# Performance work log

Measured on AMD Instinct MI355X. Metric: run time of the kernel, lower is better.

Reference implementation:

```python
import jax, jax.numpy as jnp
import numpy as np

B, L, Z, G = 512, 2713, 58, 8  # batch, chem features, seq len (zeta), d_model (gamma)
H, HD, FF, NL = 8, 1, 2048, 6  # heads, head_dim, ffn dim, layers
RNA_IN, LIN1, LIN2 = 1018, 256, 64
CAT, C1, C2 = LIN2 + Z * G, 64, 8  # 528, 64, 8


def setup_inputs() -> dict:
    key = jax.random.key(0)
    ks = iter(jax.random.split(key, 40))
    r = lambda shape, s=0.05: (jax.random.normal(next(ks), shape, dtype=jnp.float32) * s)
    inp = {
        'rna': jax.random.normal(next(ks), (B, RNA_IN), dtype=jnp.float32),
        'drug': jax.random.normal(next(ks), (B, L, Z), dtype=jnp.float32),
        'lin1_w': r((LIN1, RNA_IN)), 'lin1_b': r((LIN1,)),
        'lin2_w': r((LIN2, LIN1)), 'lin2_b': r((LIN2,)),
        'chem_w': r((G, L)),  # chem_embedding: Linear(2713->8, no bias)
        'pos_w': r((G, Z)),   # pos_embedding on one-hot == its weight columns
        'qkv_w': r((NL, 3 * G, G)), 'qkv_b': r((NL, 3 * G)),
        'out_w': r((NL, G, G)), 'out_b': r((NL, G)),
        'ln1_g': jnp.ones((NL, G), jnp.float32), 'ln1_b': jnp.zeros((NL, G), jnp.float32),
        'ff1_w': r((NL, FF, G)), 'ff1_b': r((NL, FF)),
        'ff2_w': r((NL, G, FF)), 'ff2_b': r((NL, G)),
        'ln2_g': jnp.ones((NL, G), jnp.float32), 'ln2_b': jnp.zeros((NL, G), jnp.float32),
        'c1_w': r((C1, CAT)), 'c1_b': r((C1,)),
        'c2_w': r((C2, C1)), 'c2_b': r((C2,)),
        'c3_w': r((1, C2)), 'c3_b': r((1,)),
    }
    return inp


def _layernorm(x, g, b, eps=1e-5):
    mu = jnp.mean(x, axis=-1, keepdims=True)
    var = jnp.mean(jnp.square(x - mu), axis=-1, keepdims=True)
    return (x - mu) * jax.lax.rsqrt(var + eps) * g + b


def _forward(rna, drug, lin1_w, lin1_b, lin2_w, lin2_b, chem_w, pos_w,
             qkv_w, qkv_b, out_w, out_b, ln1_g, ln1_b,
             ff1_w, ff1_b, ff2_w, ff2_b, ln2_g, ln2_b,
             c1_w, c1_b, c2_w, c2_b, c3_w, c3_b):
    # rna branch: two linear layers (no activation in original forward)
    r = rna @ lin1_w.T + lin1_b
    r = r @ lin2_w.T + lin2_b  # [B, 64]

    # Embedding: E = W_chem @ M + W_pos (the double loop, vectorized)
    E = jnp.einsum('gl,blz->bgz', chem_w, drug) + pos_w[None]  # [B, G, Z]
    x = jnp.transpose(E, (0, 2, 1))  # [B, Z, G] (batch_first transformer input)

    scale = 1.0 / np.sqrt(HD)
    for i in range(NL):  # 6 post-norm TransformerEncoderLayers, relu FFN
        qkv = x @ qkv_w[i].T + qkv_b[i]  # [B, Z, 3G]
        q, k, v = jnp.split(qkv, 3, axis=-1)
        qh = q.reshape(B, Z, H, HD)
        kh = k.reshape(B, Z, H, HD)
        vh = v.reshape(B, Z, H, HD)
        scores = jnp.einsum('bshd,bthd->bhst', qh, kh) * scale
        a = jax.nn.softmax(scores, axis=-1)
        o = jnp.einsum('bhst,bthd->bshd', a, vh).reshape(B, Z, G)
        o = o @ out_w[i].T + out_b[i]
        x = _layernorm(x + o, ln1_g[i], ln1_b[i])
        ff = jax.nn.relu(x @ ff1_w[i].T + ff1_b[i]) @ ff2_w[i].T + ff2_b[i]
        x = _layernorm(x + ff, ln2_g[i], ln2_b[i])

    flat = x.reshape(B, Z * G)  # [B, 464]
    h = jnp.concatenate([r, flat], axis=1)  # [B, 528]
    h = h @ c1_w.T + c1_b
    h = h @ c2_w.T + c2_b
    return h @ c3_w.T + c3_b  # [B, 1]


def reference(rna, drug, lin1_w, lin1_b, lin2_w, lin2_b, chem_w, pos_w,
              qkv_w, qkv_b, out_w, out_b, ln1_g, ln1_b,
              ff1_w, ff1_b, ff2_w, ff2_b, ln2_g, ln2_b,
              c1_w, c1_b, c2_w, c2_b, c3_w, c3_b):
    return _forward(rna, drug, lin1_w, lin1_b, lin2_w, lin2_b, chem_w, pos_w,
                    qkv_w, qkv_b, out_w, out_b, ln1_g, ln1_b,
                    ff1_w, ff1_b, ff2_w, ff2_b, ln2_g, ln2_b,
                    c1_w, c1_b, c2_w, c2_b, c3_w, c3_b)
```

## Files before the change

### kernel.cpp

```cpp
#include <hip/hip_runtime.h>

#define BB 512
#define LDIM 2713
#define ZDIM 58
#define GDIM 8
#define NLAYER 6
#define FFDIM 2048
#define RNAIN 1018
#define CATDIM 528
#define NCAT 1482
#define LQ 679

typedef float v2f __attribute__((ext_vector_type(2)));
typedef float f32x4 __attribute__((ext_vector_type(4)));
typedef _Float16 f16x4 __attribute__((ext_vector_type(4)));

#define OFF_WCATT  0
#define OFF_BPRIME 94848

__global__ __launch_bounds__(1024) void prep_kernel(
    const float* __restrict__ lin1_w, const float* __restrict__ lin1_b,
    const float* __restrict__ lin2_w, const float* __restrict__ lin2_b,
    const float* __restrict__ c1_w, const float* __restrict__ c1_b,
    float* __restrict__ ws) {
    __shared__ float Tm[16384];
    const int t = threadIdx.x;
    float* WcatT = ws + OFF_WCATT;

    if (blockIdx.x == 16) {
        if (t < 64) {
            float a = lin2_b[t];
            #pragma unroll 4
            for (int n = 0; n < 256; ++n) a += lin2_w[t * 256 + n] * lin1_b[n];
            Tm[t] = a;
        }
        __syncthreads();
        if (t < 64) {
            float a = c1_b[t];
            #pragma unroll 4
            for (int m = 0; m < 64; ++m) a += c1_w[t * CATDIM + m] * Tm[m];
            ws[OFF_BPRIME + t] = a;
        }
        for (int i = t; i < 464 * 64; i += 1024) {
            int kk = i >> 6, j = i & 63;
            WcatT[(RNAIN + kk) * 64 + j] = c1_w[j * CATDIM + 64 + kk];
        }
        return;
    }

    for (int i = t; i < 16384; i += 1024) {
        int n = i >> 6, j = i & 63;
        float a = 0.f;
        #pragma unroll 8
        for (int m = 0; m < 64; ++m) a += c1_w[j * CATDIM + m] * lin2_w[m * 256 + n];
        Tm[i] = a;
    }
    __syncthreads();
    const int k0 = blockIdx.x * 64;
    const int j = t & 63;
    for (int kr = t >> 6; kr < 64; kr += 16) {
        int k = k0 + kr;
        if (k >= RNAIN) break;
        float a = 0.f;
        #pragma unroll 8
        for (int n = 0; n < 256; ++n) a += Tm[n * 64 + j] * lin1_w[n * RNAIN + k];
        WcatT[k * 64 + j] = a;
    }
}

__global__ __launch_bounds__(1024, 8) void mega_kernel(
    const float* __restrict__ drug, const float* __restrict__ chem_w,
    const float* __restrict__ pos_w,
    const float* __restrict__ ff1_w, const float* __restrict__ ff2_w,
    const float* __restrict__ ff1_b,
    const float* __restrict__ qkv_w, const float* __restrict__ qkv_b,
    const float* __restrict__ out_w, const float* __restrict__ out_b,
    const float* __restrict__ ln1_g, const float* __restrict__ ln1_b,
    const float* __restrict__ ff2_b,
    const float* __restrict__ ln2_g, const float* __restrict__ ln2_b,
    const float* __restrict__ rna, const float* __restrict__ WcatT,
    const float* __restrict__ bprime,
    const float* __restrict__ c2_w, const float* __restrict__ c2_b,
    const float* __restrict__ c3_w, const float* __restrict__ c3_b,
    float* __restrict__ out) {
    __shared__ float smem[12864];
    float* cwl    = smem;
    float* part_e = smem + 5440;
    float* xs    = smem;
    float* qs    = smem + 512;
    float* ks    = smem + 992;
    float* vs    = smem + 1472;
    float* os    = smem + 1952;
    float* part  = smem + 2464;
    float* qkvws = smem + 10656;
    float* qkvbs = smem + 11808;
    float* outws = smem + 11952;
    float* outbs = smem + 12336;
    float* l1gs  = smem + 12384;
    float* l1bs  = smem + 12432;
    float* l2gs  = smem + 12480;
    float* l2bs  = smem + 12528;
    float* f2bs  = smem + 12576;
    float* h1s   = smem + 12624;
    float* h2s   = smem + 12688;

    const int b = blockIdx.x;
    const int t = threadIdx.x;
    const int w = __builtin_amdgcn_readfirstlane(t >> 6);
    const int lane = t & 63;
    const int quad = lane >> 4;
    const int i16 = lane & 15;

    {
        const int zc = (lane < ZDIM) ? lane : (ZDIM - 1);
        v2f acc0 = {0.f, 0.f}, acc1 = {0.f, 0.f}, acc2 = {0.f, 0.f}, acc3 = {0.f, 0.f};
        for (int q = 0; q < 4; ++q) {
            const int l0 = q * LQ;
            const int nrows = (LDIM - l0 < LQ) ? (LDIM - l0) : LQ;
            __syncthreads();
            #pragma unroll
            for (int g = 0; g < 8; ++g)
                for (int i = t; i < nrows; i += 1024)
                    cwl[i * 8 + g] = chem_w[g * LDIM + l0 + i];
            __syncthreads();
            const float* dp = drug + (size_t)b * (LDIM * ZDIM) + (size_t)l0 * ZDIM;
            int r0 = w * 43;
            int r1 = (r0 + 43 < nrows) ? (r0 + 43) : nrows;
            int r = r0;
            for (; r + 4 <= r1; r += 4) {
                float d0 = dp[(r + 0) * ZDIM + zc];
                float d1 = dp[(r + 1) * ZDIM + zc];
                float d2 = dp[(r + 2) * ZDIM + zc];
                float d3 = dp[(r + 3) * ZDIM + zc];
                const v2f* c0 = (const v2f*)(cwl + (r + 0) * 8);
                const v2f* c1 = (const v2f*)(cwl + (r + 1) * 8);
                const v2f* c2 = (const v2f*)(cwl + (r + 2) * 8);
                const v2f* c3 = (const v2f*)(cwl + (r + 3) * 8);
                v2f dd;
                dd = (v2f){d0, d0};
                acc0 += c0[0] * dd; acc1 += c0[1] * dd; acc2 += c0[2] * dd; acc3 += c0[3] * dd;
                dd = (v2f){d1, d1};
                acc0 += c1[0] * dd; acc1 += c1[1] * dd; acc2 += c1[2] * dd; acc3 += c1[3] * dd;
                dd = (v2f){d2, d2};
                acc0 += c2[0] * dd; acc1 += c2[1] * dd; acc2 += c2[2] * dd; acc3 += c2[3] * dd;
                dd = (v2f){d3, d3};
                acc0 += c3[0] * dd; acc1 += c3[1] * dd; acc2 += c3[2] * dd; acc3 += c3[3] * dd;
            }
            for (; r < r1; ++r) {
                float d = dp[r * ZDIM + zc];
                const v2f* cc = (const v2f*)(cwl + r * 8);
                v2f dd = {d, d};
                acc0 += cc[0] * dd; acc1 += cc[1] * dd; acc2 += cc[2] * dd; acc3 += cc[3] * dd;
            }
        }
        if (lane < ZDIM) {
            v2f* pr = (v2f*)(part_e + w * 464 + zc * 8);
            pr[0] = acc0; pr[1] = acc1; pr[2] = acc2; pr[3] = acc3;
        }
        __syncthreads();
        if (t < 512) {
            if (t < 464) {
                int z = t >> 3, g = t & 7;
                float s = pos_w[g * ZDIM + z];
                #pragma unroll
                for (int ww = 0; ww < 16; ++ww) s += part_e[ww * 464 + t];
                xs[t] = s;
            } else {
                xs[t] = 0.f;
            }
        }
        __syncthreads();
    }

    for (int i = t; i < 1152; i += 1024) qkvws[i] = qkv_w[i];
    if (t < 144) qkvbs[t] = qkv_b[t];
    if (t < 384) outws[t] = out_w[t];
    if (t < 48) {
        outbs[t] = out_b[t];
        l1gs[t] = ln1_g[t]; l1bs[t] = ln1_b[t];
        l2gs[t] = ln2_g[t]; l2bs[t] = ln2_b[t];
        f2bs[t] = ff2_b[t];
    }
    __syncthreads();

    for (int li = 0; li < NLAYER; ++li) {
        if (t < 464) {
            int z = t >> 3, h = t & 7;
            const float4* xr = (const float4*)(xs + z * 8);
            float4 x0 = xr[0], x1 = xr[1];
            #pragma unroll
            for (int p = 0; p < 3; ++p) {
                int j = p * 8 + h;
                const float4* wr = (const float4*)(qkvws + li * 192 + j * 8);
                float4 w0 = wr[0], w1 = wr[1];
                float a = qkvbs[li * 24 + j]
                        + x0.x * w0.x + x0.y * w0.y + x0.z * w0.z + x0.w * w0.w
                        + x1.x * w1.x + x1.y * w1.y + x1.z * w1.z + x1.w * w1.w;
                float* dst = (p == 0) ? qs : (p == 1) ? ks : vs;
                dst[h * 60 + z] = a;
            }
        }
        __syncthreads();

        if (t < 464) {
            int h = t & 7, s = t >> 3;
            float q = qs[h * 60 + s];
            const float4* kr = (const float4*)(ks + h * 60);
            const float4* vr = (const float4*)(vs + h * 60);
            float sum = 0.f, oa = 0.f;
            #pragma unroll 2
            for (int c = 0; c < 14; ++c) {
                float4 k4 = kr[c], v4 = vr[c];
                float e0 = __expf(q * k4.x); sum += e0; oa += e0 * v4.x;
                float e1 = __expf(q * k4.y); sum += e1; oa += e1 * v4.y;
                float e2 = __expf(q * k4.z); sum += e2; oa += e2 * v4.z;
                float e3 = __expf(q * k4.w); sum += e3; oa += e3 * v4.w;
            }
            {
                const float* kk = ks + h * 60;
                const float* vv = vs + h * 60;
                float e0 = __expf(q * kk[56]); sum += e0; oa += e0 * vv[56];
                float e1 = __expf(q * kk[57]); sum += e1; oa += e1 * vv[57];
            }
            os[t] = oa / sum;
        }
        __syncthreads();

        if (t < 464) {
            int z = t >> 3, g = t & 7;
            const float4* orow = (const float4*)(os + z * 8);
            float4 o0 = orow[0], o1 = orow[1];
            const float4* wr = (const float4*)(outws + li * 64 + g * 8);
            float4 w0 = wr[0], w1 = wr[1];
            float a = outbs[li * 8 + g] + xs[t]
                    + o0.x * w0.x + o0.y * w0.y + o0.z * w0.z + o0.w * w0.w
                    + o1.x * w1.x + o1.y * w1.y + o1.z * w1.z + o1.w * w1.w;
            float s8 = a + __shfl_xor(a, 1);
            s8 += __shfl_xor(s8, 2);
            s8 += __shfl_xor(s8, 4);
            float mu = s8 * 0.125f;
            float d = a - mu;
            float vv = d * d;
            vv += __shfl_xor(vv, 1); vv += __shfl_xor(vv, 2); vv += __shfl_xor(vv, 4);
            float inv = rsqrtf(vv * 0.125f + 1e-5f);
            xs[t] = d * inv * l1gs[li * 8 + g] + l1bs[li * 8 + g];
        }
        __syncthreads();

        {
            f16x4 xb[4];
            #pragma unroll
            for (int nt = 0; nt < 4; ++nt) {
                if (quad < 2) {
                    const float4* xp = (const float4*)(xs + (nt * 16 + i16) * 8 + quad * 4);
                    float4 xv = *xp;
                    xb[nt][0] = (_Float16)xv.x; xb[nt][1] = (_Float16)xv.y;
                    xb[nt][2] = (_Float16)xv.z; xb[nt][3] = (_Float16)xv.w;
                } else {
                    xb[nt][0] = (_Float16)0.f; xb[nt][1] = (_Float16)0.f;
                    xb[nt][2] = (_Float16)0.f; xb[nt][3] = (_Float16)0.f;
                }
            }
            f32x4 oacc[4];
            #pragma unroll
            for (int nt = 0; nt < 4; ++nt) { oacc[nt][0]=0.f; oacc[nt][1]=0.f; oacc[nt][2]=0.f; oacc[nt][3]=0.f; }

            const float* w1p = ff1_w + ((size_t)li * FFDIM + w * 128) * 8;
            const float* a2p = ff2_w + (size_t)li * GDIM * FFDIM + w * 128;
            const float* b1p = ff1_b + li * FFDIM + w * 128;

            #pragma unroll 2
            for (int ft = 0; ft < 8; ++ft) {
                f16x4 w1f = {};
                if (lane < 32) {
                    f32x4 v = *(const f32x4*)(w1p + (size_t)(ft * 16 + i16) * 8 + quad * 4);
                    w1f[0] = (_Float16)v[0]; w1f[1] = (_Float16)v[1];
                    w1f[2] = (_Float16)v[2]; w1f[3] = (_Float16)v[3];
                }
                f16x4 a2f = {};
                if (i16 < 8) {
                    f32x4 v = *(const f32x4*)(a2p + (size_t)i16 * FFDIM + ft * 16 + quad * 4);
                    a2f[0] = (_Float16)v[0]; a2f[1] = (_Float16)v[1];
                    a2f[2] = (_Float16)v[2]; a2f[3] = (_Float16)v[3];
                }
                f32x4 b1v = *(const f32x4*)(b1p + ft * 16 + quad * 4);
                #pragma unroll
                for (int nt = 0; nt < 4; ++nt) {
                    f32x4 h = b1v;
                    h = __builtin_amdgcn_mfma_f32_16x16x16f16(w1f, xb[nt], h, 0, 0, 0);
                    h[0] = fmaxf(h[0], 0.f); h[1] = fmaxf(h[1], 0.f);
                    h[2] = fmaxf(h[2], 0.f); h[3] = fmaxf(h[3], 0.f);
                    f16x4 hb;
                    hb[0] = (_Float16)h[0]; hb[1] = (_Float16)h[1];
                    hb[2] = (_Float16)h[2]; hb[3] = (_Float16)h[3];
                    oacc[nt] = __builtin_amdgcn_mfma_f32_16x16x16f16(a2f, hb, oacc[nt], 0, 0, 0);
                }
            }
            if (quad < 2) {
                #pragma unroll
                for (int nt = 0; nt < 4; ++nt) {
                    float4 o4 = make_float4(oacc[nt][0], oacc[nt][1], oacc[nt][2], oacc[nt][3]);
                    *(float4*)(part + ((w * 64 + nt * 16 + i16) * 8 + quad * 4)) = o4;
                }
            }
        }
        __syncthreads();

        if (t < 464) {
            int z = t >> 3, g = t & 7;
            float s = 0.f;
            #pragma unroll
            for (int ww = 0; ww < 16; ++ww) s += part[(ww * 64 + z) * 8 + g];
            float a = xs[t] + s + f2bs[li * 8 + g];
            float s8 = a + __shfl_xor(a, 1);
            s8 += __shfl_xor(s8, 2);
            s8 += __shfl_xor(s8, 4);
            float mu = s8 * 0.125f;
            float d = a - mu;
            float vv = d * d;
            vv += __shfl_xor(vv, 1); vv += __shfl_xor(vv, 2); vv += __shfl_xor(vv, 4);
            float inv = rsqrtf(vv * 0.125f + 1e-5f);
            xs[t] = d * inv * l2gs[li * 8 + g] + l2bs[li * 8 + g];
        }
        __syncthreads();
    }

    {
        float* cat = part;
        float* partial = part + 4096;
        const float* rg = rna + (size_t)b * RNAIN;
        for (int i = t; i < RNAIN; i += 1024) cat[i] = rg[i];
        __syncthreads();
        int j = lane;
        int k0 = w * 93;
        int k1 = (k0 + 93 < NCAT) ? (k0 + 93) : NCAT;
        float a = (w == 0) ? bprime[j] : 0.f;
        #pragma unroll 4
        for (int k = k0; k < k1; ++k) {
            float ck = (k < RNAIN) ? cat[k] : xs[k - RNAIN];
            a += ck * WcatT[k * 64 + j];
        }
        partial[w * 64 + j] = a;
        __syncthreads();
        if (t < 64) {
            float s = 0.f;
            #pragma unroll
            for (int ww = 0; ww < 16; ++ww) s += partial[ww * 64 + t];
            h1s[t] = s;
        }
    }
    __syncthreads();
    if (t < 8) {
        float a2 = c2_b[t];
        #pragma unroll 8
        for (int m = 0; m < 64; ++m) a2 += h1s[m] * c2_w[t * 64 + m];
        h2s[t] = a2;
    }
    __syncthreads();
    if (t == 0) {
        float a3 = c3_b[0];
        #pragma unroll
        for (int jj = 0; jj < 8; ++jj) a3 += h2s[jj] * c3_w[jj];
        out[b] = a3;
    }
}

extern "C" void kernel_launch(void* const* d_in, const int* in_sizes, int n_in,
                              void* d_out, int out_size, void* d_ws, size_t ws_size,
                              hipStream_t stream) {
    const float* rna    = (const float*)d_in[0];
    const float* drug   = (const float*)d_in[1];
    const float* lin1_w = (const float*)d_in[2];
    const float* lin1_b = (const float*)d_in[3];
    const float* lin2_w = (const float*)d_in[4];
    const float* lin2_b = (const float*)d_in[5];
    const float* chem_w = (const float*)d_in[6];
    const float* pos_w  = (const float*)d_in[7];
    const float* qkv_w  = (const float*)d_in[8];
    const float* qkv_b  = (const float*)d_in[9];
    const float* out_w  = (const float*)d_in[10];
    const float* out_b  = (const float*)d_in[11];
    const float* ln1_g  = (const float*)d_in[12];
    const float* ln1_b  = (const float*)d_in[13];
    const float* ff1_w  = (const float*)d_in[14];
    const float* ff1_b  = (const float*)d_in[15];
    const float* ff2_w  = (const float*)d_in[16];
    const float* ff2_b  = (const float*)d_in[17];
    const float* ln2_g  = (const float*)d_in[18];
    const float* ln2_b  = (const float*)d_in[19];
    const float* c1_w   = (const float*)d_in[20];
    const float* c1_b   = (const float*)d_in[21];
    const float* c2_w   = (const float*)d_in[22];
    const float* c2_b   = (const float*)d_in[23];
    const float* c3_w   = (const float*)d_in[24];
    const float* c3_b   = (const float*)d_in[25];
    float* ws  = (float*)d_ws;
    float* out = (float*)d_out;

    hipLaunchKernelGGL(prep_kernel, dim3(17), dim3(1024), 0, stream,
                       lin1_w, lin1_b, lin2_w, lin2_b, c1_w, c1_b, ws);
    hipLaunchKernelGGL(mega_kernel, dim3(BB), dim3(1024), 0, stream,
                       drug, chem_w, pos_w, ff1_w, ff2_w, ff1_b,
                       qkv_w, qkv_b, out_w, out_b,
                       ln1_g, ln1_b, ff2_b, ln2_g, ln2_b,
                       rna, ws + OFF_WCATT, ws + OFF_BPRIME,
                       c2_w, c2_b, c3_w, c3_b, out);
}
```

Baseline: 732.6 us.

## Halve mega_kernel block size, fuse out-proj via shuffles, restructure prep GEMMs

The main kernel now runs with 512 threads per block instead of 1024, so each wave covers twice as many embedding rows, FFN tiles and classifier inputs, and shared memory shrinks so more blocks may fit per CU. The attention output projection is folded into the softmax threads with width-8 shuffles, which removes the os buffer and one barrier per layer. The prep kernel reorders its matrix product chain: it stages an lin1 tile and a transposed c1 in shared memory and computes lin2·lin1 first. The bias path is parallelised across threads. The trade-off is more serial work per wave in the main kernel in exchange for fewer barriers and possibly higher occupancy.

Result: faster. 698.9 us (-4.6%).

```diff
diff --git a/kernel.cpp b/kernel.cpp
--- a/kernel.cpp
+++ b/kernel.cpp
@@ -23,52 +23,76 @@
     const float* __restrict__ lin2_w, const float* __restrict__ lin2_b,
     const float* __restrict__ c1_w, const float* __restrict__ c1_b,
     float* __restrict__ ws) {
-    __shared__ float Tm[16384];
+    __shared__ float lin1s[256 * 64];
+    __shared__ float Ut[64 * 64];
+    __shared__ float c1T[64 * 64];
     const int t = threadIdx.x;
     float* WcatT = ws + OFF_WCATT;
 
     if (blockIdx.x == 16) {
+        {
+            int m = t >> 4, q = t & 15;
+            float a = 0.f;
+            #pragma unroll
+            for (int nn = 0; nn < 16; ++nn)
+                a += lin2_w[m * 256 + q * 16 + nn] * lin1_b[q * 16 + nn];
+            lin1s[m * 16 + q] = a;
+        }
+        __syncthreads();
         if (t < 64) {
             float a = lin2_b[t];
-            #pragma unroll 4
-            for (int n = 0; n < 256; ++n) a += lin2_w[t * 256 + n] * lin1_b[n];
-            Tm[t] = a;
+            #pragma unroll
+            for (int q = 0; q < 16; ++q) a += lin1s[t * 16 + q];
+            Ut[t] = a;
         }
         __syncthreads();
         if (t < 64) {
             float a = c1_b[t];
-            #pragma unroll 4
-            for (int m = 0; m < 64; ++m) a += c1_w[t * CATDIM + m] * Tm[m];
+            #pragma unroll 8
+            for (int m = 0; m < 64; ++m) a += c1_w[t * CATDIM + m] * Ut[m];
             ws[OFF_BPRIME + t] = a;
         }
         for (int i = t; i < 464 * 64; i += 1024) {
-            int kk = i >> 6, j = i & 63;
+            int j = i / 464, kk = i % 464;
             WcatT[(RNAIN + kk) * 64 + j] = c1_w[j * CATDIM + 64 + kk];
         }
         return;
     }
 
-    for (int i = t; i < 16384; i += 1024) {
-        int n = i >> 6, j = i & 63;
+    const int k0 = blockIdx.x * 64;
+    const int nk = (RNAIN - k0 < 64) ? (RNAIN - k0) : 64;
+    for (int i = t; i < 256 * 64; i += 1024) {
+        int n = i >> 6, kl = i & 63;
+        lin1s[i] = (kl < nk) ? lin1_w[n * RNAIN + k0 + kl] : 0.f;
+    }
+    for (int i = t; i < 64 * 64; i += 1024) {
+        int j = i >> 6, m = i & 63;
+        c1T[m * 64 + j] = c1_w[j * CATDIM + m];
+    }
+    __syncthreads();
+    for (int mp = 0; mp < 4; ++mp) {
+        int m = (t >> 6) + mp * 16;
+        int kl = t & 63;
+        const float* l2r = lin2_w + m * 256;
         float a = 0.f;
         #pragma unroll 8
-        for (int m = 0; m < 64; ++m) a += c1_w[j * CATDIM + m] * lin2_w[m * 256 + n];
-        Tm[i] = a;
+        for (int n = 0; n < 256; ++n) a += l2r[n] * lin1s[n * 64 + kl];
+        Ut[m * 64 + kl] = a;
     }
     __syncthreads();
-    const int k0 = blockIdx.x * 64;
-    const int j = t & 63;
-    for (int kr = t >> 6; kr < 64; kr += 16) {
-        int k = k0 + kr;
-        if (k >= RNAIN) break;
-        float a = 0.f;
-        #pragma unroll 8
-        for (int n = 0; n < 256; ++n) a += Tm[n * 64 + j] * lin1_w[n * RNAIN + k];
-        WcatT[k * 64 + j] = a;
+    for (int kp = 0; kp < 4; ++kp) {
+        int kr = (t >> 6) + kp * 16;
+        int j = t & 63;
+        if (kr < nk) {
+            float a = 0.f;
+            #pragma unroll 8
+            for (int m = 0; m < 64; ++m) a += Ut[m * 64 + kr] * c1T[m * 64 + j];
+            WcatT[(k0 + kr) * 64 + j] = a;
+        }
     }
 }
 
-__global__ __launch_bounds__(1024, 8) void mega_kernel(
+__global__ __launch_bounds__(512, 8) void mega_kernel(
     const float* __restrict__ drug, const float* __restrict__ chem_w,
     const float* __restrict__ pos_w,
     const float* __restrict__ ff1_w, const float* __restrict__ ff2_w,
@@ -83,26 +107,25 @@
     const float* __restrict__ c2_w, const float* __restrict__ c2_b,
     const float* __restrict__ c3_w, const float* __restrict__ c3_b,
     float* __restrict__ out) {
-    __shared__ float smem[12864];
+    __shared__ float smem[9152];
     float* cwl    = smem;
     float* part_e = smem + 5440;
     float* xs    = smem;
     float* qs    = smem + 512;
     float* ks    = smem + 992;
     float* vs    = smem + 1472;
-    float* os    = smem + 1952;
-    float* part  = smem + 2464;
-    float* qkvws = smem + 10656;
-    float* qkvbs = smem + 11808;
-    float* outws = smem + 11952;
-    float* outbs = smem + 12336;
-    float* l1gs  = smem + 12384;
-    float* l1bs  = smem + 12432;
-    float* l2gs  = smem + 12480;
-    float* l2bs  = smem + 12528;
-    float* f2bs  = smem + 12576;
-    float* h1s   = smem + 12624;
-    float* h2s   = smem + 12688;
+    float* part  = smem + 1952;
+    float* qkvws = smem + 6048;
+    float* qkvbs = smem + 7200;
+    float* outws = smem + 7344;
+    float* outbs = smem + 7728;
+    float* l1gs  = smem + 7776;
+    float* l1bs  = smem + 7824;
+    float* l2gs  = smem + 7872;
+    float* l2bs  = smem + 7920;
+    float* f2bs  = smem + 7968;
+    float* h1s   = smem + 8016;
+    float* h2s   = smem + 8080;
 
     const int b = blockIdx.x;
     const int t = threadIdx.x;
@@ -120,12 +143,12 @@
             __syncthreads();
             #pragma unroll
             for (int g = 0; g < 8; ++g)
-                for (int i = t; i < nrows; i += 1024)
+                for (int i = t; i < nrows; i += 512)
                     cwl[i * 8 + g] = chem_w[g * LDIM + l0 + i];
             __syncthreads();
             const float* dp = drug + (size_t)b * (LDIM * ZDIM) + (size_t)l0 * ZDIM;
-            int r0 = w * 43;
-            int r1 = (r0 + 43 < nrows) ? (r0 + 43) : nrows;
+            int r0 = w * 85;
+            int r1 = (r0 + 85 < nrows) ? (r0 + 85) : nrows;
             int r = r0;
             for (; r + 4 <= r1; r += 4) {
                 float d0 = dp[(r + 0) * ZDIM + zc];
@@ -158,21 +181,19 @@
             pr[0] = acc0; pr[1] = acc1; pr[2] = acc2; pr[3] = acc3;
         }
         __syncthreads();
-        if (t < 512) {
-            if (t < 464) {
-                int z = t >> 3, g = t & 7;
-                float s = pos_w[g * ZDIM + z];
-                #pragma unroll
-                for (int ww = 0; ww < 16; ++ww) s += part_e[ww * 464 + t];
-                xs[t] = s;
-            } else {
-                xs[t] = 0.f;
-            }
-        }
-        __syncthreads();
-    }
-
-    for (int i = t; i < 1152; i += 1024) qkvws[i] = qkv_w[i];
+        if (t < 464) {
+            int z = t >> 3, g = t & 7;
+            float s = pos_w[g * ZDIM + z];
+            #pragma unroll
+            for (int ww = 0; ww < 8; ++ww) s += part_e[ww * 464 + t];
+            xs[t] = s;
+        } else if (t < 512) {
+            xs[t] = 0.f;
+        }
+        __syncthreads();
+    }
+
+    for (int i = t; i < 1152; i += 512) qkvws[i] = qkv_w[i];
     if (t < 144) qkvbs[t] = qkv_b[t];
     if (t < 384) outws[t] = out_w[t];
     if (t < 48) {
@@ -222,19 +243,13 @@
                 float e0 = __expf(q * kk[56]); sum += e0; oa += e0 * vv[56];
                 float e1 = __expf(q * kk[57]); sum += e1; oa += e1 * vv[57];
             }
-            os[t] = oa / sum;
-        }
-        __syncthreads();
-
-        if (t < 464) {
-            int z = t >> 3, g = t & 7;
-            const float4* orow = (const float4*)(os + z * 8);
-            float4 o0 = orow[0], o1 = orow[1];
-            const float4* wr = (const float4*)(outws + li * 64 + g * 8);
-            float4 w0 = wr[0], w1 = wr[1];
-            float a = outbs[li * 8 + g] + xs[t]
-                    + o0.x * w0.x + o0.y * w0.y + o0.z * w0.z + o0.w * w0.w
-                    + o1.x * w1.x + o1.y * w1.y + o1.z * w1.z + o1.w * w1.w;
+            float o = oa / sum;
+            int g = h;
+            float a = outbs[li * 8 + g] + xs[t];
+            const float* wr8 = outws + li * 64 + g * 8;
+            #pragma unroll
+            for (int hh = 0; hh < 8; ++hh)
+                a += __shfl(o, hh, 8) * wr8[hh];
             float s8 = a + __shfl_xor(a, 1);
             s8 += __shfl_xor(s8, 2);
             s8 += __shfl_xor(s8, 4);
@@ -265,12 +280,12 @@
             #pragma unroll
             for (int nt = 0; nt < 4; ++nt) { oacc[nt][0]=0.f; oacc[nt][1]=0.f; oacc[nt][2]=0.f; oacc[nt][3]=0.f; }
 
-            const float* w1p = ff1_w + ((size_t)li * FFDIM + w * 128) * 8;
-            const float* a2p = ff2_w + (size_t)li * GDIM * FFDIM + w * 128;
-            const float* b1p = ff1_b + li * FFDIM + w * 128;
+            const float* w1p = ff1_w + ((size_t)li * FFDIM + w * 256) * 8;
+            const float* a2p = ff2_w + (size_t)li * GDIM * FFDIM + w * 256;
+            const float* b1p = ff1_b + li * FFDIM + w * 256;
 
             #pragma unroll 2
-            for (int ft = 0; ft < 8; ++ft) {
+            for (int ft = 0; ft < 16; ++ft) {
                 f16x4 w1f = {};
                 if (lane < 32) {
                     f32x4 v = *(const f32x4*)(w1p + (size_t)(ft * 16 + i16) * 8 + quad * 4);
@@ -310,7 +325,7 @@
             int z = t >> 3, g = t & 7;
             float s = 0.f;
             #pragma unroll
-            for (int ww = 0; ww < 16; ++ww) s += part[(ww * 64 + z) * 8 + g];
+            for (int ww = 0; ww < 8; ++ww) s += part[(ww * 64 + z) * 8 + g];
             float a = xs[t] + s + f2bs[li * 8 + g];
             float s8 = a + __shfl_xor(a, 1);
             s8 += __shfl_xor(s8, 2);
@@ -327,13 +342,13 @@
 
     {
         float* cat = part;
-        float* partial = part + 4096;
+        float* partial = part + 1024;
         const float* rg = rna + (size_t)b * RNAIN;
-        for (int i = t; i < RNAIN; i += 1024) cat[i] = rg[i];
+        for (int i = t; i < RNAIN; i += 512) cat[i] = rg[i];
         __syncthreads();
         int j = lane;
-        int k0 = w * 93;
-        int k1 = (k0 + 93 < NCAT) ? (k0 + 93) : NCAT;
+        int k0 = w * 186;
+        int k1 = (k0 + 186 < NCAT) ? (k0 + 186) : NCAT;
         float a = (w == 0) ? bprime[j] : 0.f;
         #pragma unroll 4
         for (int k = k0; k < k1; ++k) {
@@ -345,7 +360,7 @@
         if (t < 64) {
             float s = 0.f;
             #pragma unroll
-            for (int ww = 0; ww < 16; ++ww) s += partial[ww * 64 + t];
+            for (int ww = 0; ww < 8; ++ww) s += partial[ww * 64 + t];
             h1s[t] = s;
         }
     }
@@ -399,7 +414,7 @@
 
     hipLaunchKernelGGL(prep_kernel, dim3(17), dim3(1024), 0, stream,
                        lin1_w, lin1_b, lin2_w, lin2_b, c1_w, c1_b, ws);
-    hipLaunchKernelGGL(mega_kernel, dim3(BB), dim3(1024), 0, stream,
+    hipLaunchKernelGGL(mega_kernel, dim3(BB), dim3(512), 0, stream,
                        drug, chem_w, pos_w, ff1_w, ff2_w, ff1_b,
                        qkv_w, qkv_b, out_w, out_b,
                        ln1_g, ln1_b, ff2_b, ln2_g, ln2_b,
```
